# Kernel optimization log

Measured on AMD Instinct MI355X. Metric: run time of the kernel, lower is better.

## Reference

```python
import jax, jax.numpy as jnp
import numpy as np

B, T, I, H = 256, 2048, 128, 128

def setup_inputs() -> dict:
    key = jax.random.key(0)
    k = jax.random.split(key, 5)
    bound = 1.0 / np.sqrt(H)  # torch RNNCell init: U(-1/sqrt(H), 1/sqrt(H))
    return {
        "x": jax.random.normal(k[0], (B, T, I), dtype=jnp.float32),
        "weight_ih": jax.random.uniform(k[1], (H, I), jnp.float32, -bound, bound),
        "weight_hh": jax.random.uniform(k[2], (H, H), jnp.float32, -bound, bound),
        "bias_ih": jax.random.uniform(k[3], (H,), jnp.float32, -bound, bound),
        "bias_hh": jax.random.uniform(k[4], (H,), jnp.float32, -bound, bound),
    }

def reference(x, weight_ih, weight_hh, bias_ih, bias_hh):
    # Tanh RNN: h_t = tanh(x_t @ W_ih^T + b_ih + h_{t-1} @ W_hh^T + b_hh)
    # Precompute the input projection for all timesteps (one big GEMM),
    # then scan the recurrent part (sequential dependency on h).
    b = x.shape[0]
    h0 = jnp.zeros((b, weight_hh.shape[0]), dtype=x.dtype)
    # [B, T, H]
    x_proj = jnp.einsum('bti,hi->bth', x, weight_ih) + bias_ih + bias_hh

    def step(h, xt):  # xt: [B, H]
        h_new = jnp.tanh(xt + h @ weight_hh.T)
        return h_new, h_new

    _, out = jax.lax.scan(step, h0, jnp.swapaxes(x_proj, 0, 1))  # out: [T, B, H]
    return jnp.swapaxes(out, 0, 1)  # [B, T, H]
```

## Files before the change

### kernel.cpp

```cpp
#include <hip/hip_runtime.h>

#define BB 256
#define TT 2048
#define II 128
#define HH 128
#define GS 16
#define NG (TT / GS)

typedef __attribute__((ext_vector_type(8))) short short8;
typedef __attribute__((ext_vector_type(4))) float f32x4;

__device__ __forceinline__ void step_barrier() {
    asm volatile("s_waitcnt lgkmcnt(0)\n\ts_barrier" ::: "memory");
}

__device__ __forceinline__ float tanh_fast(float s) {
#if __has_builtin(__builtin_amdgcn_exp2f)
    const float e = __builtin_amdgcn_exp2f(s * 2.8853900817779268f);
#else
    const float e = exp2f(s * 2.8853900817779268f);
#endif
    return 1.0f - 2.0f * __builtin_amdgcn_rcpf(e + 1.0f);
}

__device__ __forceinline__ unsigned int f2bf(float f) {
    unsigned int u = __float_as_uint(f);
    u += 0x7FFF + ((u >> 16) & 1);
    return u >> 16;
}
__device__ __forceinline__ unsigned int pack2(float lo, float hi) {
    return f2bf(lo) | (f2bf(hi) << 16);
}

__launch_bounds__(512, 1)
__global__ void rnn_pipe(const float* __restrict__ x,
                         const float* __restrict__ w_ih,
                         const float* __restrict__ w_hh,
                         const float* __restrict__ b_ih,
                         const float* __restrict__ b_hh,
                         float* __restrict__ out) {
    const int b    = blockIdx.x;
    const int tid  = threadIdx.x;
    const int wave = tid >> 6;
    const int lane = tid & 63;
    const bool hw  = (wave < 4);

    __shared__ __align__(16) unsigned short hA[2][HH];
    __shared__ __align__(16) float axbuf[2][GS][HH];
    __shared__ __align__(16) unsigned short xstage[2][4][64][8];

    const float* xb = x + (size_t)b * (TT * II);

    const int jb_h = (wave & 3) * 32;
    short8 WH[2][4];
    if (hw) {
#pragma unroll
        for (int nt = 0; nt < 2; ++nt) {
            const int jj = jb_h + nt * 16 + (lane & 15);
#pragma unroll
            for (int kf = 0; kf < 4; ++kf) {
                short8 s;
#pragma unroll
                for (int e = 0; e < 8; ++e) {
                    const int kp = kf * 32 + (lane >> 4) * 8 + e;
                    const int m  = kp & 31;
                    const int ko = (kp & ~31) + (m >> 1) + ((m & 1) << 4);
                    s[e] = (short)f2bf(w_hh[(size_t)jj * HH + ko]);
                }
                WH[nt][kf] = s;
            }
        }
    }

    const int xwq = wave - 4;
    const int jb  = xwq * 32;
    short8 WF[2][4];
    float biasv[2];
    const int q   = tid - 256;
    const int t_s = q >> 4;
    const int m   = q & 15;
    const int i0  = m * 8;
    const int kfs = m >> 2;
    const int lps = (m & 3) * 16 + t_s;
    if (!hw) {
#pragma unroll
        for (int nt = 0; nt < 2; ++nt) {
            const int jj = jb + nt * 16 + (lane & 15);
            biasv[nt] = b_ih[jj] + b_hh[jj];
#pragma unroll
            for (int kf = 0; kf < 4; ++kf) {
                const float* wp = w_ih + (size_t)jj * II + kf * 32 + (lane >> 4) * 8;
                short8 s;
#pragma unroll
                for (int e = 0; e < 8; ++e) s[e] = (short)f2bf(wp[e]);
                WF[nt][kf] = s;
            }
        }
    }

#define STAGE_X(BUF, R0, R1) do { \
        uint4 P_; P_.x = pack2((R0).x, (R0).y); P_.y = pack2((R0).z, (R0).w); \
        P_.z = pack2((R1).x, (R1).y); P_.w = pack2((R1).z, (R1).w); \
        *reinterpret_cast<uint4*>(&xstage[BUF][kfs][lps][0]) = P_; } while (0)

#define XPROJ(SB, AB) do { \
        const short8 A0 = *reinterpret_cast<const short8*>(&xstage[SB][0][lane][0]); \
        const short8 A1 = *reinterpret_cast<const short8*>(&xstage[SB][1][lane][0]); \
        const short8 A2 = *reinterpret_cast<const short8*>(&xstage[SB][2][lane][0]); \
        const short8 A3 = *reinterpret_cast<const short8*>(&xstage[SB][3][lane][0]); \
        f32x4 ac0 = {0.f, 0.f, 0.f, 0.f}, ac1 = {0.f, 0.f, 0.f, 0.f}; \
        ac0 = __builtin_amdgcn_mfma_f32_16x16x32_bf16(A0, WF[0][0], ac0, 0, 0, 0); \
        ac0 = __builtin_amdgcn_mfma_f32_16x16x32_bf16(A1, WF[0][1], ac0, 0, 0, 0); \
        ac0 = __builtin_amdgcn_mfma_f32_16x16x32_bf16(A2, WF[0][2], ac0, 0, 0, 0); \
        ac0 = __builtin_amdgcn_mfma_f32_16x16x32_bf16(A3, WF[0][3], ac0, 0, 0, 0); \
        ac1 = __builtin_amdgcn_mfma_f32_16x16x32_bf16(A0, WF[1][0], ac1, 0, 0, 0); \
        ac1 = __builtin_amdgcn_mfma_f32_16x16x32_bf16(A1, WF[1][1], ac1, 0, 0, 0); \
        ac1 = __builtin_amdgcn_mfma_f32_16x16x32_bf16(A2, WF[1][2], ac1, 0, 0, 0); \
        ac1 = __builtin_amdgcn_mfma_f32_16x16x32_bf16(A3, WF[1][3], ac1, 0, 0, 0); \
        const int c_ = lane & 15, rb_ = (lane >> 4) * 4; \
        _Pragma("unroll") \
        for (int r = 0; r < 4; ++r) { \
            axbuf[AB][rb_ + r][jb + c_]      = ac0[r] + biasv[0]; \
            axbuf[AB][rb_ + r][jb + 16 + c_] = ac1[r] + biasv[1]; \
        } } while (0)

    float4 nr0, nr1;
    if (!hw) {
        float4 p0 = *reinterpret_cast<const float4*>(&xb[t_s * II + i0]);
        float4 p1 = *reinterpret_cast<const float4*>(&xb[t_s * II + i0 + 4]);
        STAGE_X(1, p0, p1);
        nr0 = *reinterpret_cast<const float4*>(&xb[(GS + t_s) * II + i0]);
        nr1 = *reinterpret_cast<const float4*>(&xb[(GS + t_s) * II + i0 + 4]);
    }
    if (tid < HH) hA[0][tid] = 0;
    __syncthreads();
    if (!hw) {
        XPROJ(1, 0);
        STAGE_X(0, nr0, nr1);
    }
    __syncthreads();

    float axn0 = 0.f, axn1 = 0.f;
    if (hw) {
        axn0 = axbuf[0][0][jb_h + (lane & 15)];
        axn1 = axbuf[0][0][jb_h + 16 + (lane & 15)];
    }

    for (int g = 0; g < NG; ++g) {
#pragma unroll
        for (int w = 0; w < GS; ++w) {
            if (hw) {
                const int p  = w & 1;
                const int ko = (lane >> 4) * 8;
                const short8 A0 = *reinterpret_cast<const short8*>(&hA[p][ 0 + ko]);
                const short8 A1 = *reinterpret_cast<const short8*>(&hA[p][32 + ko]);
                const short8 A2 = *reinterpret_cast<const short8*>(&hA[p][64 + ko]);
                const short8 A3 = *reinterpret_cast<const short8*>(&hA[p][96 + ko]);
                f32x4 a0 = {0.f,0.f,0.f,0.f}, a1 = {0.f,0.f,0.f,0.f};
                f32x4 a2 = {0.f,0.f,0.f,0.f}, a3 = {0.f,0.f,0.f,0.f};
                f32x4 c0 = {0.f,0.f,0.f,0.f}, c1 = {0.f,0.f,0.f,0.f};
                f32x4 c2 = {0.f,0.f,0.f,0.f}, c3 = {0.f,0.f,0.f,0.f};
                a0 = __builtin_amdgcn_mfma_f32_16x16x32_bf16(A0, WH[0][0], a0, 0, 0, 0);
                a1 = __builtin_amdgcn_mfma_f32_16x16x32_bf16(A1, WH[0][1], a1, 0, 0, 0);
                a2 = __builtin_amdgcn_mfma_f32_16x16x32_bf16(A2, WH[0][2], a2, 0, 0, 0);
                a3 = __builtin_amdgcn_mfma_f32_16x16x32_bf16(A3, WH[0][3], a3, 0, 0, 0);
                c0 = __builtin_amdgcn_mfma_f32_16x16x32_bf16(A0, WH[1][0], c0, 0, 0, 0);
                c1 = __builtin_amdgcn_mfma_f32_16x16x32_bf16(A1, WH[1][1], c1, 0, 0, 0);
                c2 = __builtin_amdgcn_mfma_f32_16x16x32_bf16(A2, WH[1][2], c2, 0, 0, 0);
                c3 = __builtin_amdgcn_mfma_f32_16x16x32_bf16(A3, WH[1][3], c3, 0, 0, 0);
                const float axv0 = axn0, axv1 = axn1;
                {
                    const int wn  = (w + 1) & (GS - 1);
                    const int gnb = (w == GS - 1) ? ((g + 1) & 1) : (g & 1);
                    axn0 = axbuf[gnb][wn][jb_h + (lane & 15)];
                    axn1 = axbuf[gnb][wn][jb_h + 16 + (lane & 15)];
                }
                const float s0 = (a0[0] + a1[0]) + (a2[0] + a3[0]) + axv0;
                const float s1 = (c0[0] + c1[0]) + (c2[0] + c3[0]) + axv1;
                const float hn0 = tanh_fast(s0);
                const float hn1 = tanh_fast(s1);
                if (lane < 16) {
                    *reinterpret_cast<unsigned int*>(&hA[p ^ 1][jb_h + 2 * lane])
                        = pack2(hn0, hn1);
                    float* ob = out + (size_t)b * (TT * HH)
                              + (size_t)(g * GS + w) * HH + jb_h + lane;
                    ob[0]  = hn0;
                    ob[16] = hn1;
                }
            } else {
                if (w == 0 && g + 1 < NG) {
                    XPROJ(g & 1, (g + 1) & 1);
                }
                if (w == 1 && g + 2 < NG) {
                    const int tb = (g + 2) * GS;
                    nr0 = *reinterpret_cast<const float4*>(&xb[(size_t)(tb + t_s) * II + i0]);
                    nr1 = *reinterpret_cast<const float4*>(&xb[(size_t)(tb + t_s) * II + i0 + 4]);
                }
                if (w == 8 && g + 2 < NG) {
                    STAGE_X((g + 1) & 1, nr0, nr1);
                }
            }
            step_barrier();
        }
    }
#undef XPROJ
#undef STAGE_X
}

extern "C" void kernel_launch(void* const* d_in, const int* in_sizes, int n_in,
                              void* d_out, int out_size, void* d_ws, size_t ws_size,
                              hipStream_t stream) {
    const float* x    = (const float*)d_in[0];
    const float* w_ih = (const float*)d_in[1];
    const float* w_hh = (const float*)d_in[2];
    const float* b_ih = (const float*)d_in[3];
    const float* b_hh = (const float*)d_in[4];
    float* out = (float*)d_out;

    rnn_pipe<<<BB, 512, 0, stream>>>(x, w_ih, w_hh, b_ih, b_hh, out);
}
```

Before: 518.8 us.

## Merge producer and recurrent waves into a single 4-wave block

Removes the warp specialization in which 4 waves ran the recurrence and 4 separate waves computed the input projection. Each of the 4 waves now does both jobs: it issues the x projection, the global x prefetch and the LDS staging at fixed steps of the group, alongside its recurrent MFMAs. This halves the threads taking part in each per-step barrier and cuts register and launch overhead. The cost is that the projection work now sits on the critical recurrent path at step 0 of every group, which may lengthen those steps.

```diff
diff --git a/kernel.cpp b/kernel.cpp
--- a/kernel.cpp
+++ b/kernel.cpp
@@ -32,7 +32,7 @@
     return f2bf(lo) | (f2bf(hi) << 16);
 }
 
-__launch_bounds__(512, 1)
+__launch_bounds__(256, 1)
 __global__ void rnn_pipe(const float* __restrict__ x,
                          const float* __restrict__ w_ih,
                          const float* __restrict__ w_hh,
@@ -43,7 +43,7 @@
     const int tid  = threadIdx.x;
     const int wave = tid >> 6;
     const int lane = tid & 63;
-    const bool hw  = (wave < 4);
+    const int jb   = wave * 32;
 
     __shared__ __align__(16) unsigned short hA[2][HH];
     __shared__ __align__(16) float axbuf[2][GS][HH];
@@ -51,52 +51,45 @@
 
     const float* xb = x + (size_t)b * (TT * II);
 
-    const int jb_h = (wave & 3) * 32;
     short8 WH[2][4];
-    if (hw) {
-#pragma unroll
-        for (int nt = 0; nt < 2; ++nt) {
-            const int jj = jb_h + nt * 16 + (lane & 15);
-#pragma unroll
-            for (int kf = 0; kf < 4; ++kf) {
-                short8 s;
-#pragma unroll
-                for (int e = 0; e < 8; ++e) {
-                    const int kp = kf * 32 + (lane >> 4) * 8 + e;
-                    const int m  = kp & 31;
-                    const int ko = (kp & ~31) + (m >> 1) + ((m & 1) << 4);
-                    s[e] = (short)f2bf(w_hh[(size_t)jj * HH + ko]);
-                }
-                WH[nt][kf] = s;
-            }
+#pragma unroll
+    for (int nt = 0; nt < 2; ++nt) {
+        const int jj = jb + nt * 16 + (lane & 15);
+#pragma unroll
+        for (int kf = 0; kf < 4; ++kf) {
+            short8 s;
+#pragma unroll
+            for (int e = 0; e < 8; ++e) {
+                const int kp = kf * 32 + (lane >> 4) * 8 + e;
+                const int mm = kp & 31;
+                const int ko = (kp & ~31) + (mm >> 1) + ((mm & 1) << 4);
+                s[e] = (short)f2bf(w_hh[(size_t)jj * HH + ko]);
+            }
+            WH[nt][kf] = s;
         }
     }
 
-    const int xwq = wave - 4;
-    const int jb  = xwq * 32;
     short8 WF[2][4];
     float biasv[2];
-    const int q   = tid - 256;
-    const int t_s = q >> 4;
-    const int m   = q & 15;
+#pragma unroll
+    for (int nt = 0; nt < 2; ++nt) {
+        const int jj = jb + nt * 16 + (lane & 15);
+        biasv[nt] = b_ih[jj] + b_hh[jj];
+#pragma unroll
+        for (int kf = 0; kf < 4; ++kf) {
+            const float* wp = w_ih + (size_t)jj * II + kf * 32 + (lane >> 4) * 8;
+            short8 s;
+#pragma unroll
+            for (int e = 0; e < 8; ++e) s[e] = (short)f2bf(wp[e]);
+            WF[nt][kf] = s;
+        }
+    }
+
+    const int t_s = tid >> 4;
+    const int m   = tid & 15;
     const int i0  = m * 8;
     const int kfs = m >> 2;
     const int lps = (m & 3) * 16 + t_s;
-    if (!hw) {
-#pragma unroll
-        for (int nt = 0; nt < 2; ++nt) {
-            const int jj = jb + nt * 16 + (lane & 15);
-            biasv[nt] = b_ih[jj] + b_hh[jj];
-#pragma unroll
-            for (int kf = 0; kf < 4; ++kf) {
-                const float* wp = w_ih + (size_t)jj * II + kf * 32 + (lane >> 4) * 8;
-                short8 s;
-#pragma unroll
-                for (int e = 0; e < 8; ++e) s[e] = (short)f2bf(wp[e]);
-                WF[nt][kf] = s;
-            }
-        }
-    }
 
 #define STAGE_X(BUF, R0, R1) do { \
         uint4 P_; P_.x = pack2((R0).x, (R0).y); P_.y = pack2((R0).z, (R0).w); \
@@ -104,19 +97,19 @@
         *reinterpret_cast<uint4*>(&xstage[BUF][kfs][lps][0]) = P_; } while (0)
 
 #define XPROJ(SB, AB) do { \
-        const short8 A0 = *reinterpret_cast<const short8*>(&xstage[SB][0][lane][0]); \
-        const short8 A1 = *reinterpret_cast<const short8*>(&xstage[SB][1][lane][0]); \
-        const short8 A2 = *reinterpret_cast<const short8*>(&xstage[SB][2][lane][0]); \
-        const short8 A3 = *reinterpret_cast<const short8*>(&xstage[SB][3][lane][0]); \
+        const short8 XA0 = *reinterpret_cast<const short8*>(&xstage[SB][0][lane][0]); \
+        const short8 XA1 = *reinterpret_cast<const short8*>(&xstage[SB][1][lane][0]); \
+        const short8 XA2 = *reinterpret_cast<const short8*>(&xstage[SB][2][lane][0]); \
+        const short8 XA3 = *reinterpret_cast<const short8*>(&xstage[SB][3][lane][0]); \
         f32x4 ac0 = {0.f, 0.f, 0.f, 0.f}, ac1 = {0.f, 0.f, 0.f, 0.f}; \
-        ac0 = __builtin_amdgcn_mfma_f32_16x16x32_bf16(A0, WF[0][0], ac0, 0, 0, 0); \
-        ac0 = __builtin_amdgcn_mfma_f32_16x16x32_bf16(A1, WF[0][1], ac0, 0, 0, 0); \
-        ac0 = __builtin_amdgcn_mfma_f32_16x16x32_bf16(A2, WF[0][2], ac0, 0, 0, 0); \
-        ac0 = __builtin_amdgcn_mfma_f32_16x16x32_bf16(A3, WF[0][3], ac0, 0, 0, 0); \
-        ac1 = __builtin_amdgcn_mfma_f32_16x16x32_bf16(A0, WF[1][0], ac1, 0, 0, 0); \
-        ac1 = __builtin_amdgcn_mfma_f32_16x16x32_bf16(A1, WF[1][1], ac1, 0, 0, 0); \
-        ac1 = __builtin_amdgcn_mfma_f32_16x16x32_bf16(A2, WF[1][2], ac1, 0, 0, 0); \
-        ac1 = __builtin_amdgcn_mfma_f32_16x16x32_bf16(A3, WF[1][3], ac1, 0, 0, 0); \
+        ac0 = __builtin_amdgcn_mfma_f32_16x16x32_bf16(XA0, WF[0][0], ac0, 0, 0, 0); \
+        ac0 = __builtin_amdgcn_mfma_f32_16x16x32_bf16(XA1, WF[0][1], ac0, 0, 0, 0); \
+        ac0 = __builtin_amdgcn_mfma_f32_16x16x32_bf16(XA2, WF[0][2], ac0, 0, 0, 0); \
+        ac0 = __builtin_amdgcn_mfma_f32_16x16x32_bf16(XA3, WF[0][3], ac0, 0, 0, 0); \
+        ac1 = __builtin_amdgcn_mfma_f32_16x16x32_bf16(XA0, WF[1][0], ac1, 0, 0, 0); \
+        ac1 = __builtin_amdgcn_mfma_f32_16x16x32_bf16(XA1, WF[1][1], ac1, 0, 0, 0); \
+        ac1 = __builtin_amdgcn_mfma_f32_16x16x32_bf16(XA2, WF[1][2], ac1, 0, 0, 0); \
+        ac1 = __builtin_amdgcn_mfma_f32_16x16x32_bf16(XA3, WF[1][3], ac1, 0, 0, 0); \
         const int c_ = lane & 15, rb_ = (lane >> 4) * 4; \
         _Pragma("unroll") \
         for (int r = 0; r < 4; ++r) { \
@@ -125,7 +118,7 @@
         } } while (0)
 
     float4 nr0, nr1;
-    if (!hw) {
+    {
         float4 p0 = *reinterpret_cast<const float4*>(&xb[t_s * II + i0]);
         float4 p1 = *reinterpret_cast<const float4*>(&xb[t_s * II + i0 + 4]);
         STAGE_X(1, p0, p1);
@@ -134,72 +127,70 @@
     }
     if (tid < HH) hA[0][tid] = 0;
     __syncthreads();
-    if (!hw) {
-        XPROJ(1, 0);
-        STAGE_X(0, nr0, nr1);
-    }
+    XPROJ(1, 0);
+    STAGE_X(0, nr0, nr1);
     __syncthreads();
 
-    float axn0 = 0.f, axn1 = 0.f;
-    if (hw) {
-        axn0 = axbuf[0][0][jb_h + (lane & 15)];
-        axn1 = axbuf[0][0][jb_h + 16 + (lane & 15)];
-    }
+    const int c16 = lane & 15;
+    float axn0 = axbuf[0][0][jb + c16];
+    float axn1 = axbuf[0][0][jb + 16 + c16];
+
+    float* ob = out + (size_t)b * (TT * HH) + jb + lane;
 
     for (int g = 0; g < NG; ++g) {
 #pragma unroll
         for (int w = 0; w < GS; ++w) {
-            if (hw) {
-                const int p  = w & 1;
-                const int ko = (lane >> 4) * 8;
-                const short8 A0 = *reinterpret_cast<const short8*>(&hA[p][ 0 + ko]);
-                const short8 A1 = *reinterpret_cast<const short8*>(&hA[p][32 + ko]);
-                const short8 A2 = *reinterpret_cast<const short8*>(&hA[p][64 + ko]);
-                const short8 A3 = *reinterpret_cast<const short8*>(&hA[p][96 + ko]);
-                f32x4 a0 = {0.f,0.f,0.f,0.f}, a1 = {0.f,0.f,0.f,0.f};
-                f32x4 a2 = {0.f,0.f,0.f,0.f}, a3 = {0.f,0.f,0.f,0.f};
-                f32x4 c0 = {0.f,0.f,0.f,0.f}, c1 = {0.f,0.f,0.f,0.f};
-                f32x4 c2 = {0.f,0.f,0.f,0.f}, c3 = {0.f,0.f,0.f,0.f};
-                a0 = __builtin_amdgcn_mfma_f32_16x16x32_bf16(A0, WH[0][0], a0, 0, 0, 0);
-                a1 = __builtin_amdgcn_mfma_f32_16x16x32_bf16(A1, WH[0][1], a1, 0, 0, 0);
-                a2 = __builtin_amdgcn_mfma_f32_16x16x32_bf16(A2, WH[0][2], a2, 0, 0, 0);
-                a3 = __builtin_amdgcn_mfma_f32_16x16x32_bf16(A3, WH[0][3], a3, 0, 0, 0);
-                c0 = __builtin_amdgcn_mfma_f32_16x16x32_bf16(A0, WH[1][0], c0, 0, 0, 0);
-                c1 = __builtin_amdgcn_mfma_f32_16x16x32_bf16(A1, WH[1][1], c1, 0, 0, 0);
-                c2 = __builtin_amdgcn_mfma_f32_16x16x32_bf16(A2, WH[1][2], c2, 0, 0, 0);
-                c3 = __builtin_amdgcn_mfma_f32_16x16x32_bf16(A3, WH[1][3], c3, 0, 0, 0);
-                const float axv0 = axn0, axv1 = axn1;
-                {
-                    const int wn  = (w + 1) & (GS - 1);
-                    const int gnb = (w == GS - 1) ? ((g + 1) & 1) : (g & 1);
-                    axn0 = axbuf[gnb][wn][jb_h + (lane & 15)];
-                    axn1 = axbuf[gnb][wn][jb_h + 16 + (lane & 15)];
-                }
-                const float s0 = (a0[0] + a1[0]) + (a2[0] + a3[0]) + axv0;
-                const float s1 = (c0[0] + c1[0]) + (c2[0] + c3[0]) + axv1;
-                const float hn0 = tanh_fast(s0);
-                const float hn1 = tanh_fast(s1);
-                if (lane < 16) {
-                    *reinterpret_cast<unsigned int*>(&hA[p ^ 1][jb_h + 2 * lane])
-                        = pack2(hn0, hn1);
-                    float* ob = out + (size_t)b * (TT * HH)
-                              + (size_t)(g * GS + w) * HH + jb_h + lane;
-                    ob[0]  = hn0;
-                    ob[16] = hn1;
-                }
-            } else {
-                if (w == 0 && g + 1 < NG) {
-                    XPROJ(g & 1, (g + 1) & 1);
-                }
-                if (w == 1 && g + 2 < NG) {
-                    const int tb = (g + 2) * GS;
-                    nr0 = *reinterpret_cast<const float4*>(&xb[(size_t)(tb + t_s) * II + i0]);
-                    nr1 = *reinterpret_cast<const float4*>(&xb[(size_t)(tb + t_s) * II + i0 + 4]);
-                }
-                if (w == 8 && g + 2 < NG) {
-                    STAGE_X((g + 1) & 1, nr0, nr1);
-                }
-            }
+            const int p  = w & 1;
+            const int ko = (lane >> 4) * 8;
+            const short8 A0 = *reinterpret_cast<const short8*>(&hA[p][ 0 + ko]);
+            const short8 A1 = *reinterpret_cast<const short8*>(&hA[p][32 + ko]);
+            const short8 A2 = *reinterpret_cast<const short8*>(&hA[p][64 + ko]);
+            const short8 A3 = *reinterpret_cast<const short8*>(&hA[p][96 + ko]);
+
+            if (w == 0 && g + 1 < NG) {
+                XPROJ(g & 1, (g + 1) & 1);
+            }
+            if (w == 1 && g + 2 < NG) {
+                const int tb = (g + 2) * GS;
+                nr0 = *reinterpret_cast<const float4*>(&xb[(size_t)(tb + t_s) * II + i0]);
+                nr1 = *reinterpret_cast<const float4*>(&xb[(size_t)(tb + t_s) * II + i0 + 4]);
+            }
+            if (w == 8 && g + 2 < NG) {
+                STAGE_X((g + 1) & 1, nr0, nr1);
+            }
+
+            f32x4 a0 = {0.f,0.f,0.f,0.f}, a1 = {0.f,0.f,0.f,0.f};
+            f32x4 a2 = {0.f,0.f,0.f,0.f}, a3 = {0.f,0.f,0.f,0.f};
+            f32x4 c0 = {0.f,0.f,0.f,0.f}, c1 = {0.f,0.f,0.f,0.f};
+            f32x4 c2 = {0.f,0.f,0.f,0.f}, c3 = {0.f,0.f,0.f,0.f};
+            a0 = __builtin_amdgcn_mfma_f32_16x16x32_bf16(A0, WH[0][0], a0, 0, 0, 0);
+            a1 = __builtin_amdgcn_mfma_f32_16x16x32_bf16(A1, WH[0][1], a1, 0, 0, 0);
+            a2 = __builtin_amdgcn_mfma_f32_16x16x32_bf16(A2, WH[0][2], a2, 0, 0, 0);
+            a3 = __builtin_amdgcn_mfma_f32_16x16x32_bf16(A3, WH[0][3], a3, 0, 0, 0);
+            c0 = __builtin_amdgcn_mfma_f32_16x16x32_bf16(A0, WH[1][0], c0, 0, 0, 0);
+            c1 = __builtin_amdgcn_mfma_f32_16x16x32_bf16(A1, WH[1][1], c1, 0, 0, 0);
+            c2 = __builtin_amdgcn_mfma_f32_16x16x32_bf16(A2, WH[1][2], c2, 0, 0, 0);
+            c3 = __builtin_amdgcn_mfma_f32_16x16x32_bf16(A3, WH[1][3], c3, 0, 0, 0);
+
+            const float axv0 = axn0, axv1 = axn1;
+            {
+                const int wn  = (w + 1) & (GS - 1);
+                const int gnb = (w == GS - 1) ? ((g + 1) & 1) : (g & 1);
+                axn0 = axbuf[gnb][wn][jb + c16];
+                axn1 = axbuf[gnb][wn][jb + 16 + c16];
+            }
+
+            const float s0 = (a0[0] + a1[0]) + (a2[0] + a3[0]) + axv0;
+            const float s1 = (c0[0] + c1[0]) + (c2[0] + c3[0]) + axv1;
+            const float hn0 = tanh_fast(s0);
+            const float hn1 = tanh_fast(s1);
+            if (lane < 16) {
+                *reinterpret_cast<unsigned int*>(&hA[p ^ 1][jb + 2 * lane])
+                    = pack2(hn0, hn1);
+                ob[0]  = hn0;
+                ob[16] = hn1;
+            }
+            ob += HH;
             step_barrier();
         }
     }
@@ -217,5 +208,5 @@
     const float* b_hh = (const float*)d_in[4];
     float* out = (float*)d_out;
 
-    rnn_pipe<<<BB, 512, 0, stream>>>(x, w_ih, w_hh, b_ih, b_hh, out);
-}
+    rnn_pipe<<<BB, 256, 0, stream>>>(x, w_ih, w_hh, b_ih, b_hh, out);
+}
```

New measurement: 556.5 us. 7.3% more time.

## Spread input-projection MFMAs across steps and fold bias and ax into accumulators

Applied to the files above, without the earlier changes.

The producer waves no longer run the whole 8-MFMA input projection in one step. They load the A fragments at step 0, issue one MFMA per step over steps 1-8 into independent accumulators seeded with the bias, and write the summed result at step 9, so no single barrier interval carries a long producer burst. The recurrent waves seed the first MFMA accumulator with the precomputed ax value instead of adding it after the MFMAs, and the output pointer is advanced incrementally rather than recomputed each step. The staging write moves to step 11 so the staging buffer is not overwritten before its fragments are consumed. The cost is more live registers in the producer waves and more branching inside the unrolled loop.

```diff
diff --git a/kernel.cpp b/kernel.cpp
--- a/kernel.cpp
+++ b/kernel.cpp
@@ -50,6 +50,7 @@
     __shared__ __align__(16) unsigned short xstage[2][4][64][8];
 
     const float* xb = x + (size_t)b * (TT * II);
+    const f32x4 z4 = {0.f, 0.f, 0.f, 0.f};
 
     const int jb_h = (wave & 3) * 32;
     short8 WH[2][4];
@@ -63,8 +64,8 @@
 #pragma unroll
                 for (int e = 0; e < 8; ++e) {
                     const int kp = kf * 32 + (lane >> 4) * 8 + e;
-                    const int m  = kp & 31;
-                    const int ko = (kp & ~31) + (m >> 1) + ((m & 1) << 4);
+                    const int mm = kp & 31;
+                    const int ko = (kp & ~31) + (mm >> 1) + ((mm & 1) << 4);
                     s[e] = (short)f2bf(w_hh[(size_t)jj * HH + ko]);
                 }
                 WH[nt][kf] = s;
@@ -76,6 +77,7 @@
     const int jb  = xwq * 32;
     short8 WF[2][4];
     float biasv[2];
+    f32x4 bs0 = z4, bs1 = z4;
     const int q   = tid - 256;
     const int t_s = q >> 4;
     const int m   = q & 15;
@@ -96,6 +98,8 @@
                 WF[nt][kf] = s;
             }
         }
+#pragma unroll
+        for (int r = 0; r < 4; ++r) { bs0[r] = biasv[0]; bs1[r] = biasv[1]; }
     }
 
 #define STAGE_X(BUF, R0, R1) do { \
@@ -104,19 +108,19 @@
         *reinterpret_cast<uint4*>(&xstage[BUF][kfs][lps][0]) = P_; } while (0)
 
 #define XPROJ(SB, AB) do { \
-        const short8 A0 = *reinterpret_cast<const short8*>(&xstage[SB][0][lane][0]); \
-        const short8 A1 = *reinterpret_cast<const short8*>(&xstage[SB][1][lane][0]); \
-        const short8 A2 = *reinterpret_cast<const short8*>(&xstage[SB][2][lane][0]); \
-        const short8 A3 = *reinterpret_cast<const short8*>(&xstage[SB][3][lane][0]); \
-        f32x4 ac0 = {0.f, 0.f, 0.f, 0.f}, ac1 = {0.f, 0.f, 0.f, 0.f}; \
-        ac0 = __builtin_amdgcn_mfma_f32_16x16x32_bf16(A0, WF[0][0], ac0, 0, 0, 0); \
-        ac0 = __builtin_amdgcn_mfma_f32_16x16x32_bf16(A1, WF[0][1], ac0, 0, 0, 0); \
-        ac0 = __builtin_amdgcn_mfma_f32_16x16x32_bf16(A2, WF[0][2], ac0, 0, 0, 0); \
-        ac0 = __builtin_amdgcn_mfma_f32_16x16x32_bf16(A3, WF[0][3], ac0, 0, 0, 0); \
-        ac1 = __builtin_amdgcn_mfma_f32_16x16x32_bf16(A0, WF[1][0], ac1, 0, 0, 0); \
-        ac1 = __builtin_amdgcn_mfma_f32_16x16x32_bf16(A1, WF[1][1], ac1, 0, 0, 0); \
-        ac1 = __builtin_amdgcn_mfma_f32_16x16x32_bf16(A2, WF[1][2], ac1, 0, 0, 0); \
-        ac1 = __builtin_amdgcn_mfma_f32_16x16x32_bf16(A3, WF[1][3], ac1, 0, 0, 0); \
+        const short8 PA0 = *reinterpret_cast<const short8*>(&xstage[SB][0][lane][0]); \
+        const short8 PA1 = *reinterpret_cast<const short8*>(&xstage[SB][1][lane][0]); \
+        const short8 PA2 = *reinterpret_cast<const short8*>(&xstage[SB][2][lane][0]); \
+        const short8 PA3 = *reinterpret_cast<const short8*>(&xstage[SB][3][lane][0]); \
+        f32x4 ac0 = z4, ac1 = z4; \
+        ac0 = __builtin_amdgcn_mfma_f32_16x16x32_bf16(PA0, WF[0][0], ac0, 0, 0, 0); \
+        ac0 = __builtin_amdgcn_mfma_f32_16x16x32_bf16(PA1, WF[0][1], ac0, 0, 0, 0); \
+        ac0 = __builtin_amdgcn_mfma_f32_16x16x32_bf16(PA2, WF[0][2], ac0, 0, 0, 0); \
+        ac0 = __builtin_amdgcn_mfma_f32_16x16x32_bf16(PA3, WF[0][3], ac0, 0, 0, 0); \
+        ac1 = __builtin_amdgcn_mfma_f32_16x16x32_bf16(PA0, WF[1][0], ac1, 0, 0, 0); \
+        ac1 = __builtin_amdgcn_mfma_f32_16x16x32_bf16(PA1, WF[1][1], ac1, 0, 0, 0); \
+        ac1 = __builtin_amdgcn_mfma_f32_16x16x32_bf16(PA2, WF[1][2], ac1, 0, 0, 0); \
+        ac1 = __builtin_amdgcn_mfma_f32_16x16x32_bf16(PA3, WF[1][3], ac1, 0, 0, 0); \
         const int c_ = lane & 15, rb_ = (lane >> 4) * 4; \
         _Pragma("unroll") \
         for (int r = 0; r < 4; ++r) { \
@@ -140,11 +144,18 @@
     }
     __syncthreads();
 
+    const int c16 = lane & 15;
     float axn0 = 0.f, axn1 = 0.f;
+    f32x4 d00 = z4, d10 = z4;
+    float* ob = out + (size_t)b * (TT * HH) + jb_h + lane;
     if (hw) {
-        axn0 = axbuf[0][0][jb_h + (lane & 15)];
-        axn1 = axbuf[0][0][jb_h + 16 + (lane & 15)];
-    }
+        axn0 = axbuf[0][0][jb_h + c16];
+        axn1 = axbuf[0][0][jb_h + 16 + c16];
+    }
+
+    short8 XA0 = {}, XA1 = {}, XA2 = {}, XA3 = {};
+    f32x4 xp0 = z4, xp1 = z4, xp2 = z4, xp3 = z4;
+    f32x4 yp0 = z4, yp1 = z4, yp2 = z4, yp3 = z4;
 
     for (int g = 0; g < NG; ++g) {
 #pragma unroll
@@ -156,47 +167,67 @@
                 const short8 A1 = *reinterpret_cast<const short8*>(&hA[p][32 + ko]);
                 const short8 A2 = *reinterpret_cast<const short8*>(&hA[p][64 + ko]);
                 const short8 A3 = *reinterpret_cast<const short8*>(&hA[p][96 + ko]);
-                f32x4 a0 = {0.f,0.f,0.f,0.f}, a1 = {0.f,0.f,0.f,0.f};
-                f32x4 a2 = {0.f,0.f,0.f,0.f}, a3 = {0.f,0.f,0.f,0.f};
-                f32x4 c0 = {0.f,0.f,0.f,0.f}, c1 = {0.f,0.f,0.f,0.f};
-                f32x4 c2 = {0.f,0.f,0.f,0.f}, c3 = {0.f,0.f,0.f,0.f};
-                a0 = __builtin_amdgcn_mfma_f32_16x16x32_bf16(A0, WH[0][0], a0, 0, 0, 0);
-                a1 = __builtin_amdgcn_mfma_f32_16x16x32_bf16(A1, WH[0][1], a1, 0, 0, 0);
-                a2 = __builtin_amdgcn_mfma_f32_16x16x32_bf16(A2, WH[0][2], a2, 0, 0, 0);
-                a3 = __builtin_amdgcn_mfma_f32_16x16x32_bf16(A3, WH[0][3], a3, 0, 0, 0);
-                c0 = __builtin_amdgcn_mfma_f32_16x16x32_bf16(A0, WH[1][0], c0, 0, 0, 0);
-                c1 = __builtin_amdgcn_mfma_f32_16x16x32_bf16(A1, WH[1][1], c1, 0, 0, 0);
-                c2 = __builtin_amdgcn_mfma_f32_16x16x32_bf16(A2, WH[1][2], c2, 0, 0, 0);
-                c3 = __builtin_amdgcn_mfma_f32_16x16x32_bf16(A3, WH[1][3], c3, 0, 0, 0);
-                const float axv0 = axn0, axv1 = axn1;
+                d00[0] = axn0;
+                d10[0] = axn1;
+                f32x4 e01, e02, e03, e11, e12, e13;
+                d00 = __builtin_amdgcn_mfma_f32_16x16x32_bf16(A0, WH[0][0], d00, 0, 0, 0);
+                e01 = __builtin_amdgcn_mfma_f32_16x16x32_bf16(A1, WH[0][1], z4,  0, 0, 0);
+                e02 = __builtin_amdgcn_mfma_f32_16x16x32_bf16(A2, WH[0][2], z4,  0, 0, 0);
+                e03 = __builtin_amdgcn_mfma_f32_16x16x32_bf16(A3, WH[0][3], z4,  0, 0, 0);
+                d10 = __builtin_amdgcn_mfma_f32_16x16x32_bf16(A0, WH[1][0], d10, 0, 0, 0);
+                e11 = __builtin_amdgcn_mfma_f32_16x16x32_bf16(A1, WH[1][1], z4,  0, 0, 0);
+                e12 = __builtin_amdgcn_mfma_f32_16x16x32_bf16(A2, WH[1][2], z4,  0, 0, 0);
+                e13 = __builtin_amdgcn_mfma_f32_16x16x32_bf16(A3, WH[1][3], z4,  0, 0, 0);
                 {
                     const int wn  = (w + 1) & (GS - 1);
                     const int gnb = (w == GS - 1) ? ((g + 1) & 1) : (g & 1);
-                    axn0 = axbuf[gnb][wn][jb_h + (lane & 15)];
-                    axn1 = axbuf[gnb][wn][jb_h + 16 + (lane & 15)];
-                }
-                const float s0 = (a0[0] + a1[0]) + (a2[0] + a3[0]) + axv0;
-                const float s1 = (c0[0] + c1[0]) + (c2[0] + c3[0]) + axv1;
+                    axn0 = axbuf[gnb][wn][jb_h + c16];
+                    axn1 = axbuf[gnb][wn][jb_h + 16 + c16];
+                }
+                const float s0 = (d00[0] + e01[0]) + (e02[0] + e03[0]);
+                const float s1 = (d10[0] + e11[0]) + (e12[0] + e13[0]);
                 const float hn0 = tanh_fast(s0);
                 const float hn1 = tanh_fast(s1);
                 if (lane < 16) {
                     *reinterpret_cast<unsigned int*>(&hA[p ^ 1][jb_h + 2 * lane])
                         = pack2(hn0, hn1);
-                    float* ob = out + (size_t)b * (TT * HH)
-                              + (size_t)(g * GS + w) * HH + jb_h + lane;
                     ob[0]  = hn0;
                     ob[16] = hn1;
                 }
+                ob += HH;
             } else {
                 if (w == 0 && g + 1 < NG) {
-                    XPROJ(g & 1, (g + 1) & 1);
+                    XA0 = *reinterpret_cast<const short8*>(&xstage[g & 1][0][lane][0]);
+                    XA1 = *reinterpret_cast<const short8*>(&xstage[g & 1][1][lane][0]);
+                    XA2 = *reinterpret_cast<const short8*>(&xstage[g & 1][2][lane][0]);
+                    XA3 = *reinterpret_cast<const short8*>(&xstage[g & 1][3][lane][0]);
                 }
                 if (w == 1 && g + 2 < NG) {
                     const int tb = (g + 2) * GS;
                     nr0 = *reinterpret_cast<const float4*>(&xb[(size_t)(tb + t_s) * II + i0]);
                     nr1 = *reinterpret_cast<const float4*>(&xb[(size_t)(tb + t_s) * II + i0 + 4]);
                 }
-                if (w == 8 && g + 2 < NG) {
+                if (g + 1 < NG) {
+                    if (w == 1) xp0 = __builtin_amdgcn_mfma_f32_16x16x32_bf16(XA0, WF[0][0], bs0, 0, 0, 0);
+                    if (w == 2) yp0 = __builtin_amdgcn_mfma_f32_16x16x32_bf16(XA0, WF[1][0], bs1, 0, 0, 0);
+                    if (w == 3) xp1 = __builtin_amdgcn_mfma_f32_16x16x32_bf16(XA1, WF[0][1], z4, 0, 0, 0);
+                    if (w == 4) yp1 = __builtin_amdgcn_mfma_f32_16x16x32_bf16(XA1, WF[1][1], z4, 0, 0, 0);
+                    if (w == 5) xp2 = __builtin_amdgcn_mfma_f32_16x16x32_bf16(XA2, WF[0][2], z4, 0, 0, 0);
+                    if (w == 6) yp2 = __builtin_amdgcn_mfma_f32_16x16x32_bf16(XA2, WF[1][2], z4, 0, 0, 0);
+                    if (w == 7) xp3 = __builtin_amdgcn_mfma_f32_16x16x32_bf16(XA3, WF[0][3], z4, 0, 0, 0);
+                    if (w == 8) yp3 = __builtin_amdgcn_mfma_f32_16x16x32_bf16(XA3, WF[1][3], z4, 0, 0, 0);
+                    if (w == 9) {
+                        const f32x4 t0 = (xp0 + xp1) + (xp2 + xp3);
+                        const f32x4 t1 = (yp0 + yp1) + (yp2 + yp3);
+                        const int c_ = lane & 15, rb_ = (lane >> 4) * 4;
+#pragma unroll
+                        for (int r = 0; r < 4; ++r) {
+                            axbuf[(g + 1) & 1][rb_ + r][jb + c_]      = t0[r];
+                            axbuf[(g + 1) & 1][rb_ + r][jb + 16 + c_] = t1[r];
+                        }
+                    }
+                }
+                if (w == 11 && g + 2 < NG) {
                     STAGE_X((g + 1) & 1, nr0, nr1);
                 }
             }
```

Result: no change. 512.6 us (-1.2%).
